# Kernel optimization log

Measured on AMD Instinct MI355X. Metric: run time of the kernel, lower is better.

Reference implementation:

```python
import jax, jax.numpy as jnp
import numpy as np

MODEL = 2048
LATENT = 512
POS = 1024
NH = 16
HD = MODEL // NH        # 128
PHD = POS // NH         # 64
THETA = 50000.0


def _rope_tables(S, dim, base=THETA):
    inv_freq = 1.0 / (base ** (jnp.arange(0, dim, 2, dtype=jnp.float32) / dim))
    t = jnp.arange(S, dtype=jnp.float32)
    freqs = jnp.outer(t, inv_freq)                  # [S, dim/2]
    emb = jnp.concatenate([freqs, freqs], axis=-1)  # [S, dim]
    return jnp.cos(emb), jnp.sin(emb)


def _rotate_half(x):
    h = x.shape[-1] // 2
    return jnp.concatenate([-x[..., h:], x[..., :h]], axis=-1)


def _apply_rope(x, cos, sin):
    # x: [..., S, dim]; cos/sin: [S, dim]
    return x * cos + _rotate_half(x) * sin


def setup_inputs() -> dict:
    key = jax.random.key(0)
    ks = jax.random.split(key, 16)
    std = 0.02
    d = {
        'x':      jax.random.normal(ks[0], (2, 2048, MODEL), jnp.float32),
        'w_qkv':  jax.random.normal(ks[1], (MODEL, 3 * LATENT), jnp.float32) * std,
        'b_qkv':  jnp.zeros((3 * LATENT,), jnp.float32),
        'w_qup':  jax.random.normal(ks[2], (LATENT, MODEL), jnp.float32) * std,
        'b_qup':  jnp.zeros((MODEL,), jnp.float32),
        'w_kup':  jax.random.normal(ks[3], (LATENT, MODEL), jnp.float32) * std,
        'b_kup':  jnp.zeros((MODEL,), jnp.float32),
        'w_vup':  jax.random.normal(ks[4], (LATENT, MODEL), jnp.float32) * std,
        'b_vup':  jnp.zeros((MODEL,), jnp.float32),
        'w_qpos': jax.random.normal(ks[5], (LATENT, POS), jnp.float32) * std,
        'b_qpos': jnp.zeros((POS,), jnp.float32),
        'w_kpos': jax.random.normal(ks[6], (MODEL, PHD), jnp.float32) * std,
        'b_kpos': jnp.zeros((PHD,), jnp.float32),
        'w_o':    jax.random.normal(ks[7], (MODEL, MODEL), jnp.float32) * std,
        'b_o':    jnp.zeros((MODEL,), jnp.float32),
    }
    return d


def reference(x, w_qkv, b_qkv, w_qup, b_qup, w_kup, b_kup, w_vup, b_vup,
              w_qpos, b_qpos, w_kpos, b_kpos, w_o, b_o):
    B, S, _ = x.shape
    # fused down-projection into shared latent
    latent_qkv = x @ w_qkv + b_qkv                       # [B,S,3L]
    lq, lk, lv = jnp.split(latent_qkv, 3, axis=-1)       # each [B,S,L]

    cos, sin = _rope_tables(S, PHD)

    # decoupled positional key (shared across heads), RoPE on sub-slice
    pos_k = x @ w_kpos + b_kpos                          # [B,S,PHD]
    pos_k = _apply_rope(pos_k, cos, sin)

    # up-projections
    q = (lq @ w_qup + b_qup).reshape(B, S, NH, HD).transpose(0, 2, 1, 3)
    k = (lk @ w_kup + b_kup).reshape(B, S, NH, HD).transpose(0, 2, 1, 3)
    v = (lv @ w_vup + b_vup).reshape(B, S, NH, HD).transpose(0, 2, 1, 3)

    pos_q = (lq @ w_qpos + b_qpos).reshape(B, S, NH, PHD).transpose(0, 2, 1, 3)
    pos_q = _apply_rope(pos_q, cos, sin)                 # [B,NH,S,PHD]

    pos_kh = jnp.broadcast_to(pos_k[:, None], (B, NH, S, PHD))
    q = jnp.concatenate([q, pos_q], axis=-1)             # [B,NH,S,HD+PHD]
    k = jnp.concatenate([k, pos_kh], axis=-1)

    scale = 1.0 / jnp.sqrt(jnp.asarray(HD + PHD, x.dtype))
    scores = jnp.einsum('bhqd,bhkd->bhqk', q, k) * scale
    causal = jnp.tril(jnp.ones((S, S), bool))
    scores = jnp.where(causal, scores, jnp.finfo(scores.dtype).min)
    p = jax.nn.softmax(scores, axis=-1)
    attn = jnp.einsum('bhqk,bhkd->bhqd', p, v)           # [B,NH,S,HD]
    attn = attn.transpose(0, 2, 1, 3).reshape(B, S, MODEL)
    return attn @ w_o + b_o
```

## Files before the change

### kernel.cpp

```cpp
#include <hip/hip_runtime.h>
#include <cstdint>
#include <cstddef>

typedef __bf16 bf16x8 __attribute__((ext_vector_type(8)));
typedef float  f32x4  __attribute__((ext_vector_type(4)));
typedef unsigned short us8 __attribute__((ext_vector_type(8)));
typedef unsigned short us4 __attribute__((ext_vector_type(4)));

__device__ __forceinline__ unsigned short f2bf(float f) {
  union { float f; unsigned u; } v; v.f = f;
  unsigned r = v.u + 0x7FFFu + ((v.u >> 16) & 1u);
  return (unsigned short)(r >> 16);
}
__device__ __forceinline__ float b2f(unsigned short h) {
  union { unsigned u; float f; } v; v.u = ((unsigned)h) << 16;
  return v.f;
}
__device__ __forceinline__ f32x4 mfma16(bf16x8 a, bf16x8 b, f32x4 c) {
  return __builtin_amdgcn_mfma_f32_16x16x32_bf16(a, b, c, 0, 0, 0);
}
__device__ __forceinline__ void gl_lds16(const unsigned short* g, unsigned short* l) {
  __builtin_amdgcn_global_load_lds(
      (const __attribute__((address_space(1))) void*)g,
      (__attribute__((address_space(3))) void*)l, 16, 0, 0);
}

__global__ void prep_all_kernel(const float* __restrict__ b_qkv,
                                const float* __restrict__ b_kpos,
                                const float* __restrict__ b_qup,
                                const float* __restrict__ b_qpos,
                                float* __restrict__ bias1,
                                float* __restrict__ bias2q,
                                float* __restrict__ costab,
                                float* __restrict__ sintab,
                                unsigned short* __restrict__ wB1,
                                const float* __restrict__ w_qkv,
                                const float* __restrict__ w_kpos,
                                const float* __restrict__ w_qup,
                                const float* __restrict__ w_qpos,
                                const float* __restrict__ w_kup,
                                const float* __restrict__ w_vup,
                                const float* __restrict__ w_o,
                                unsigned short* __restrict__ wB2q,
                                unsigned short* __restrict__ wB2k,
                                unsigned short* __restrict__ wB2v,
                                unsigned short* __restrict__ wBo,
                                int* __restrict__ counters) {
  __shared__ float tile[32][33];
  int blk = blockIdx.x;
  if (blk < 512) {
    int i = blk * 256 + threadIdx.x;
    if (i < 65536) {
      int s = i >> 5, f = i & 31;
      float inv = powf(50000.0f, -(float)f / 32.0f);
      float a = (float)s * inv;
      costab[i] = cosf(a);
      sintab[i] = sinf(a);
    }
    if (i < 2048) bias1[i] = (i < 1536) ? b_qkv[i] : (i < 1600 ? b_kpos[i - 1536] : 0.0f);
    if (i < 3072) bias2q[i] = (i < 2048) ? b_qup[i] : b_qpos[i - 2048];
    for (int jj = 0; jj < 7; ++jj)
      wB1[(size_t)1600 * 2048 + (size_t)jj * 131072 + i] = 0;
    if (i < 64) counters[i] = 0;
    return;
  }
  const float* in;
  unsigned short* out;
  int ldin, ldo, nx, j;
  if (blk < 3584)      { j = blk - 512;  in = w_qkv;  ldin = 1536; out = wB1;                        ldo = 2048; nx = 48; }
  else if (blk < 3712) { j = blk - 3584; in = w_kpos; ldin = 64;   out = wB1 + (size_t)1536 * 2048;  ldo = 2048; nx = 2;  }
  else if (blk < 4736) { j = blk - 3712; in = w_qup;  ldin = 2048; out = wB2q;                       ldo = 512;  nx = 64; }
  else if (blk < 5248) { j = blk - 4736; in = w_qpos; ldin = 1024; out = wB2q + (size_t)2048 * 512;  ldo = 512;  nx = 32; }
  else if (blk < 6272) { j = blk - 5248; in = w_kup;  ldin = 2048; out = wB2k;                       ldo = 512;  nx = 64; }
  else if (blk < 7296) { j = blk - 6272; in = w_vup;  ldin = 2048; out = wB2v;                       ldo = 512;  nx = 64; }
  else                 { j = blk - 7296; in = w_o;    ldin = 2048; out = wBo;                        ldo = 2048; nx = 64; }
  int c0 = (j % nx) * 32, r0 = (j / nx) * 32;
  int tx = threadIdx.x & 31, ty = threadIdx.x >> 5;
  for (int jj = 0; jj < 4; ++jj)
    tile[ty + jj * 8][tx] = in[(size_t)(r0 + ty + jj * 8) * ldin + c0 + tx];
  __syncthreads();
  for (int jj = 0; jj < 4; ++jj)
    out[(size_t)(c0 + ty + jj * 8) * ldo + r0 + tx] = f2bf(tile[tx][ty + jj * 8]);
}

__device__ __forceinline__ void xcd_decode(int nx, int& bx, int& by) {
  int bid = blockIdx.x, nwg = gridDim.x;
  int cpx = nwg >> 3;
  int wg = (bid & 7) * cpx + (bid >> 3);
  bx = wg % nx;
  by = wg / nx;
}

template <int OUT_MODE>
__global__ __launch_bounds__(256, 2)
void gemm_bt_kernel(const unsigned short* __restrict__ A, int lda,
                    const unsigned short* __restrict__ Bt, int ldb,
                    void* __restrict__ Cout, int ldc,
                    const float* __restrict__ bias, int K, int nx) {
  __shared__ unsigned short smem[32768];
  int tid = threadIdx.x;
  int wave = tid >> 6, lane = tid & 63;
  int g = lane >> 4, r = lane & 15;
  int wr = wave >> 1, wc = wave & 1;
  int bx, by;
  xcd_decode(nx, bx, by);
  long brow = (long)by * 128, bcol = (long)bx * 128;

  int srowl = lane >> 3;
  int sw = ((lane & 7) ^ (srowl & 7)) * 8;
  const unsigned short* Abase = A + (brow + wave * 32 + srowl) * (long)lda + sw;
  const unsigned short* Bbase = Bt + (bcol + wave * 32 + srowl) * (long)ldb + sw;

  f32x4 acc[4][4];
  for (int mi = 0; mi < 4; ++mi)
    for (int ni = 0; ni < 4; ++ni)
      acc[mi][ni] = f32x4{0.f, 0.f, 0.f, 0.f};

  auto stage = [&](int buf, int k0) {
    unsigned short* ab = smem + buf * 16384;
    unsigned short* bb = ab + 8192;
    for (int c = 0; c < 4; ++c) {
      gl_lds16(Abase + (size_t)c * 8 * lda + k0, ab + (wave * 32 + c * 8) * 64);
      gl_lds16(Bbase + (size_t)c * 8 * ldb + k0, bb + (wave * 32 + c * 8) * 64);
    }
  };

  int rx = (r & 7) << 4;
  int nt = K >> 6;

  stage(0, 0);
  for (int t = 0; t < nt; ++t) {
    if (t + 1 < nt) {
      stage((t + 1) & 1, (t + 1) << 6);
      asm volatile("s_waitcnt vmcnt(8)" ::: "memory");
    } else {
      asm volatile("s_waitcnt vmcnt(0)" ::: "memory");
    }
    __builtin_amdgcn_sched_barrier(0);
    __builtin_amdgcn_s_barrier();
    __builtin_amdgcn_sched_barrier(0);
    const char* Ab = (const char*)(smem + (t & 1) * 16384);
    const char* Bb = Ab + 16384;
    for (int kk = 0; kk < 2; ++kk) {
      bf16x8 af[4], bfv[4];
      for (int mi = 0; mi < 4; ++mi)
        af[mi] = *(const bf16x8*)(Ab + (size_t)(wr * 64 + mi * 16 + r) * 128 +
                                  ((kk * 64 + g * 16) ^ rx));
      for (int ni = 0; ni < 4; ++ni)
        bfv[ni] = *(const bf16x8*)(Bb + (size_t)(wc * 64 + ni * 16 + r) * 128 +
                                   ((kk * 64 + g * 16) ^ rx));
      for (int mi = 0; mi < 4; ++mi)
        for (int ni = 0; ni < 4; ++ni)
          acc[mi][ni] = mfma16(af[mi], bfv[ni], acc[mi][ni]);
    }
    __builtin_amdgcn_sched_barrier(0);
    __builtin_amdgcn_s_barrier();
  }

  if (OUT_MODE == 2) {
    for (int mi = 0; mi < 4; ++mi)
      for (int ni = 0; ni < 4; ++ni) {
        int col = wc * 64 + ni * 16 + r;
        float bv = bias[bcol + col];
        int rowb = wr * 64 + mi * 16 + g * 4;
        for (int i = 0; i < 4; ++i)
          smem[col * 136 + rowb + i] = f2bf(acc[mi][ni][i] + bv);
      }
    __syncthreads();
    int col = tid >> 1, half = tid & 1;
    int bh = (int)(brow >> 11) * 16 + (int)(bcol >> 7);
    unsigned short* outp = (unsigned short*)Cout +
                           ((size_t)bh * 128 + col) * 2048 + (brow & 2047);
    for (int j = 0; j < 8; ++j) {
      int row0 = half * 64 + j * 8;
      *(us8*)(outp + row0) = *(const us8*)&smem[col * 136 + row0];
    }
    return;
  }

  for (int mi = 0; mi < 4; ++mi)
    for (int ni = 0; ni < 4; ++ni) {
      long col = bcol + wc * 64 + ni * 16 + r;
      float bv = bias ? bias[col] : 0.0f;
      long rowb = brow + wr * 64 + mi * 16 + g * 4;
      for (int i = 0; i < 4; ++i) {
        float v = acc[mi][ni][i] + bv;
        if (OUT_MODE == 1)
          ((float*)Cout)[(rowb + i) * (long)ldc + col] = v;
        else
          ((unsigned short*)Cout)[(rowb + i) * (long)ldc + col] = f2bf(v);
      }
    }
}

__global__ __launch_bounds__(256, 2)
void gemm_a32_kernel(const float* __restrict__ A, int lda,
                     const unsigned short* __restrict__ Bt, int ldb,
                     unsigned short* __restrict__ Cout, int ldc,
                     const float* __restrict__ bias, int K, int nx) {
  __shared__ unsigned short smem[32768];
  int tid = threadIdx.x;
  int wave = tid >> 6, lane = tid & 63;
  int g = lane >> 4, r = lane & 15;
  int wr = wave >> 1, wc = wave & 1;
  int bx, by;
  xcd_decode(nx, bx, by);
  long brow = (long)by * 128, bcol = (long)bx * 128;

  int f4c = tid & 15, row0 = tid >> 4;
  int ablk = f4c >> 1, asub = (f4c & 1) * 8;
  const float4* Ag = (const float4*)(A + (brow + row0) * (size_t)lda) + f4c;

  int srowl = lane >> 3;
  int sw = ((lane & 7) ^ (srowl & 7)) * 8;
  const unsigned short* Bbase = Bt + (bcol + wave * 32 + srowl) * (long)ldb + sw;

  f32x4 acc[4][4];
  for (int mi = 0; mi < 4; ++mi)
    for (int ni = 0; ni < 4; ++ni)
      acc[mi][ni] = f32x4{0.f, 0.f, 0.f, 0.f};

  auto stage_b = [&](int buf, int k0) {
    unsigned short* bb = smem + 16384 + buf * 8192;
    for (int c = 0; c < 4; ++c)
      gl_lds16(Bbase + (size_t)c * 8 * ldb + k0, bb + (wave * 32 + c * 8) * 64);
  };

  int rx = (r & 7) << 4;
  int nt = K >> 6;

  float4 areg[8];
#pragma unroll
  for (int s = 0; s < 8; ++s) areg[s] = Ag[(size_t)s * 8192];
  stage_b(0, 0);

  for (int t = 0; t < nt; ++t) {
    char* alds = (char*)(smem + (t & 1) * 8192);
#pragma unroll
    for (int s = 0; s < 8; ++s) {
      us4 hv;
      hv[0] = f2bf(areg[s].x); hv[1] = f2bf(areg[s].y);
      hv[2] = f2bf(areg[s].z); hv[3] = f2bf(areg[s].w);
      int row = row0 + s * 16;
      *(us4*)(alds + row * 128 + ((ablk ^ (row & 7)) << 4) + asub) = hv;
    }
    asm volatile("s_waitcnt vmcnt(0)" ::: "memory");
    asm volatile("s_waitcnt lgkmcnt(0)" ::: "memory");
    __builtin_amdgcn_sched_barrier(0);
    __builtin_amdgcn_s_barrier();
    __builtin_amdgcn_sched_barrier(0);
    if (t + 1 < nt) {
      int k1 = (t + 1) << 6;
#pragma unroll
      for (int s = 0; s < 8; ++s) areg[s] = Ag[(size_t)s * 8192 + (k1 >> 2)];
      stage_b((t + 1) & 1, k1);
    }
    const char* Ab = (const char*)(smem + (t & 1) * 8192);
    const char* Bb = (const char*)(smem + 16384 + (t & 1) * 8192);
    for (int kk = 0; kk < 2; ++kk) {
      bf16x8 af[4], bfv[4];
      for (int mi = 0; mi < 4; ++mi)
        af[mi] = *(const bf16x8*)(Ab + (size_t)(wr * 64 + mi * 16 + r) * 128 +
                                  ((kk * 64 + g * 16) ^ rx));
      for (int ni = 0; ni < 4; ++ni)
        bfv[ni] = *(const bf16x8*)(Bb + (size_t)(wc * 64 + ni * 16 + r) * 128 +
                                   ((kk * 64 + g * 16) ^ rx));
      for (int mi = 0; mi < 4; ++mi)
        for (int ni = 0; ni < 4; ++ni)
          acc[mi][ni] = mfma16(af[mi], bfv[ni], acc[mi][ni]);
    }
    __builtin_amdgcn_sched_barrier(0);
    __builtin_amdgcn_s_barrier();
  }

  for (int mi = 0; mi < 4; ++mi)
    for (int ni = 0; ni < 4; ++ni) {
      long col = bcol + wc * 64 + ni * 16 + r;
      float bv = bias[col];
      long rowb = brow + wr * 64 + mi * 16 + g * 4;
      for (int i = 0; i < 4; ++i)
        Cout[(rowb + i) * (long)ldc + col] = f2bf(acc[mi][ni][i] + bv);
    }
}

__global__ void rope_kernel(const unsigned short* __restrict__ tmp_q,
                            const unsigned short* __restrict__ latext,
                            const float* __restrict__ costab,
                            const float* __restrict__ sintab,
                            unsigned short* __restrict__ posqr,
                            unsigned short* __restrict__ poskr) {
  int idx = blockIdx.x * 256 + threadIdx.x;
  const unsigned short* src;
  unsigned short* dst;
  int s, dp0;
  if (idx < 524288) {
    int rowA = idx >> 7, rem = idx & 127;
    int h = rem >> 3;
    dp0 = (rem & 7) * 8;
    s = rowA & 2047;
    src = tmp_q + (size_t)rowA * 3072 + 2048 + h * 64;
    dst = posqr + (size_t)rowA * 1024 + h * 64 + dp0;
  } else if (idx < 557056) {
    int j = idx - 524288;
    int rowA = j >> 3;
    dp0 = (j & 7) * 8;
    s = rowA & 2047;
    src = latext + (size_t)rowA * 2048 + 1536;
    dst = poskr + (size_t)rowA * 64 + dp0;
  } else {
    return;
  }
  us8 x1 = *(const us8*)(src + dp0);
  us8 x2 = *(const us8*)(src + (dp0 ^ 32));
  int f0 = dp0 & 31;
  const float* cp = costab + s * 32 + f0;
  const float* sp = sintab + s * 32 + f0;
  bool low = dp0 < 32;
  us8 o;
  for (int e = 0; e < 8; ++e) {
    float a = b2f(x1[e]), b = b2f(x2[e]);
    float v = low ? (a * cp[e] - b * sp[e]) : (a * cp[e] + b * sp[e]);
    o[e] = f2bf(v);
  }
  *(us8*)dst = o;
}

__device__ __forceinline__ void task_decode(int t, int& qt, int& seg, int& bh) {
  if (t < 1024) {
    qt = 31 - (t >> 7); int rem = t & 127; seg = rem >> 5; bh = rem & 31;
  } else if (t < 1792) {
    int t2 = t - 1024; int qi = t2 / 96; int rem = t2 - qi * 96;
    qt = 23 - qi; seg = rem >> 5; bh = rem & 31;
  } else if (t < 2304) {
    int t3 = t - 1792; qt = 15 - (t3 >> 6); int rem = t3 & 63; seg = rem >> 5; bh = rem & 31;
  } else {
    int t4 = t - 2304; qt = 7 - (t4 >> 5); seg = 0; bh = t4 & 31;
  }
}
__device__ __forceinline__ int task_slot(int qt, int seg, int bh) {
  if (qt >= 24) return (31 - qt) * 128 + seg * 32 + bh;
  if (qt >= 16) return 1024 + (23 - qt) * 96 + seg * 32 + bh;
  return 1792 + (15 - qt) * 64 + seg * 32 + bh;
}

__global__ __launch_bounds__(256, 2)
void flash_kernel(const unsigned short* __restrict__ tmp_q,
                  const unsigned short* __restrict__ tmp_k,
                  const unsigned short* __restrict__ posqr,
                  const unsigned short* __restrict__ poskr,
                  const unsigned short* __restrict__ vT,
                  unsigned short* __restrict__ ob,
                  unsigned short* __restrict__ Opart,
                  float* __restrict__ mlbuf,
                  int* __restrict__ counter) {
  const int S = 2048;
  int tid = threadIdx.x, wave = tid >> 6, lane = tid & 63;
  int g = lane >> 4, r = lane & 15;
  const float sl2 = 1.44269504f / 13.8564064605510183f;
  const float DEFER = 96.0f;

  __shared__ unsigned short Klds[32 * 192];
  __shared__ unsigned short Vlds[128 * 32];
  __shared__ unsigned short Plds[4][16][40];
  __shared__ int s_tile;
  char* Kb = (char*)Klds;
  char* Vb = (char*)Vlds;
  int rx7 = (r & 7) << 4, rx3 = (r & 3) << 4;

  us8 onesu;
  for (int e = 0; e < 8; ++e) onesu[e] = 0x3F80;
  bf16x8 ones = *(const bf16x8*)&onesu;

  int kn_row[2], kn_seg[2];
  for (int j = 0; j < 2; ++j) {
    int slot = j * 256 + tid;
    kn_row[j] = slot >> 4;
    kn_seg[j] = slot & 15;
  }
  int kr_row = tid >> 3, kr_seg = tid & 7;
  int v_row[2], v_seg[2];
  for (int j = 0; j < 2; ++j) {
    int slot = j * 256 + tid;
    v_row[j] = slot >> 2;
    v_seg[j] = slot & 3;
  }

  for (;;) {
    if (tid == 0) s_tile = atomicAdd(counter, 1);
    __syncthreads();
    int t = s_tile;
    if (t >= 2560) return;
    int qt, seg, bh;
    task_decode(t, qt, seg, bh);
    int b = bh >> 4, h = bh & 15;
    int qbase = qt * 64;
    int cbeg = seg * 16;
    int cend = min(cbeg + 16, 2 * (qt + 1));
    size_t rb = (size_t)b * 2048;

    const unsigned short* kpn = tmp_k + rb * 2048 + h * 128;
    const unsigned short* kpr = poskr + rb * 64;
    const unsigned short* vp = vT + (size_t)bh * 128 * S;

    bf16x8 qf[6];
    {
      size_t qrowA = rb + qbase + wave * 16 + r;
      const unsigned short* qn = tmp_q + qrowA * 3072 + h * 128 + g * 8;
      for (int c = 0; c < 4; ++c) qf[c] = *(const bf16x8*)(qn + c * 32);
      const unsigned short* qr_ = posqr + qrowA * 1024 + h * 64 + g * 8;
      qf[4] = *(const bf16x8*)(qr_);
      qf[5] = *(const bf16x8*)(qr_ + 32);
    }

    f32x4 acc[8];
    for (int d = 0; d < 8; ++d) acc[d] = f32x4{0.f, 0.f, 0.f, 0.f};
    f32x4 lacc = {0.f, 0.f, 0.f, 0.f};
    float m_r[4];
    for (int i = 0; i < 4; ++i) m_r[i] = -3.0e38f;

    us8 kreg[2], krope, vreg[2];
    {
      int kv0 = cbeg * 32;
      for (int j = 0; j < 2; ++j)
        kreg[j] = *(const us8*)(kpn + (size_t)(kv0 + kn_row[j]) * 2048 + kn_seg[j] * 8);
      krope = *(const us8*)(kpr + (size_t)(kv0 + kr_row) * 64 + kr_seg * 8);
      for (int j = 0; j < 2; ++j)
        vreg[j] = *(const us8*)(vp + (size_t)v_row[j] * S + kv0 + v_seg[j] * 8);
    }

    for (int ch = cbeg; ch < cend; ++ch) {
      for (int j = 0; j < 2; ++j)
        *(us8*)(Kb + (size_t)kn_row[j] * 384 +
                ((kn_seg[j] ^ (kn_row[j] & 7)) << 4)) = kreg[j];
      *(us8*)(Kb + (size_t)kr_row * 384 +
              (((16 + kr_seg) ^ (kr_row & 7)) << 4)) = krope;
      for (int j = 0; j < 2; ++j)
        *(us8*)(Vb + (size_t)v_row[j] * 64 +
                ((v_seg[j] ^ (v_row[j] & 3)) << 4)) = vreg[j];
      asm volatile("s_waitcnt lgkmcnt(0)" ::: "memory");
      __builtin_amdgcn_sched_barrier(0);
      __builtin_amdgcn_s_barrier();
      __builtin_amdgcn_sched_barrier(0);
      if (ch + 1 < cend) {
        int kv1 = (ch + 1) * 32;
        for (int j = 0; j < 2; ++j)
          kreg[j] = *(const us8*)(kpn + (size_t)(kv1 + kn_row[j]) * 2048 + kn_seg[j] * 8);
        krope = *(const us8*)(kpr + (size_t)(kv1 + kr_row) * 64 + kr_seg * 8);
        for (int j = 0; j < 2; ++j)
          vreg[j] = *(const us8*)(vp + (size_t)v_row[j] * S + kv1 + v_seg[j] * 8);
      }
      int kv0 = ch * 32;

      f32x4 sc0 = {0.f, 0.f, 0.f, 0.f}, sc1 = {0.f, 0.f, 0.f, 0.f};
      __builtin_amdgcn_s_setprio(1);
      for (int c = 0; c < 6; ++c) {
        bf16x8 kf0 = *(const bf16x8*)(Kb + (size_t)r * 384 + (((c * 4 + g) << 4) ^ rx7));
        sc0 = mfma16(qf[c], kf0, sc0);
      }
      for (int c = 0; c < 6; ++c) {
        bf16x8 kf1 = *(const bf16x8*)(Kb + (size_t)(16 + r) * 384 + (((c * 4 + g) << 4) ^ rx7));
        sc1 = mfma16(qf[c], kf1, sc1);
      }
      __builtin_amdgcn_s_setprio(0);

      int qi_min = qbase + wave * 16;
      if (kv0 + 31 > qi_min) {
        int kj0 = kv0 + r, kj1 = kv0 + 16 + r;
        int qi0 = qi_min + g * 4;
        for (int i = 0; i < 4; ++i) {
          if (kj0 > qi0 + i) sc0[i] = -1e30f;
          if (kj1 > qi0 + i) sc1[i] = -1e30f;
        }
      }

      float tl[4];
      bool ok = true;
      for (int i = 0; i < 4; ++i) {
        tl[i] = fmaxf(sc0[i], sc1[i]);
        ok = ok && (tl[i] - m_r[i] <= DEFER);
      }
      if (!__all(ok)) {
        for (int i = 0; i < 4; ++i) {
          float tm = tl[i];
          for (int off = 1; off < 16; off <<= 1) tm = fmaxf(tm, __shfl_xor(tm, off, 64));
          float mnew = fmaxf(m_r[i], tm);
          float corr = exp2f((m_r[i] - mnew) * sl2);
          lacc[i] *= corr;
          for (int d = 0; d < 8; ++d) acc[d][i] *= corr;
          m_r[i] = mnew;
        }
      }
      float p0[4], p1[4];
      for (int i = 0; i < 4; ++i) {
        p0[i] = exp2f((sc0[i] - m_r[i]) * sl2);
        p1[i] = exp2f((sc1[i] - m_r[i]) * sl2);
      }

      for (int i = 0; i < 4; ++i) {
        Plds[wave][g * 4 + i][r] = f2bf(p0[i]);
        Plds[wave][g * 4 + i][16 + r] = f2bf(p1[i]);
      }
      bf16x8 pa = *(const bf16x8*)&Plds[wave][r][g * 8];
      __builtin_amdgcn_s_setprio(1);
      lacc = mfma16(pa, ones, lacc);
      for (int dt = 0; dt < 8; ++dt) {
        bf16x8 vf = *(const bf16x8*)(Vb + (size_t)(dt * 16 + r) * 64 + ((g << 4) ^ rx3));
        acc[dt] = mfma16(pa, vf, acc[dt]);
      }
      __builtin_amdgcn_s_setprio(0);
      __builtin_amdgcn_sched_barrier(0);
      __builtin_amdgcn_s_barrier();
    }

    if (qt <= 7) {
      for (int i = 0; i < 4; ++i) {
        float inv = 1.0f / lacc[i];
        int row = qbase + wave * 16 + g * 4 + i;
        size_t base = (rb + row) * 2048 + h * 128;
        for (int dt = 0; dt < 8; ++dt)
          ob[base + dt * 16 + r] = f2bf(acc[dt][i] * inv);
      }
    } else {
      unsigned short* op = Opart + (size_t)t * 8192;
      for (int i = 0; i < 4; ++i) {
        int row = wave * 16 + g * 4 + i;
        for (int dt = 0; dt < 8; ++dt)
          op[row * 128 + dt * 16 + r] = f2bf(acc[dt][i]);
        if (r == 0) {
          mlbuf[(size_t)t * 128 + row * 2]     = m_r[i];
          mlbuf[(size_t)t * 128 + row * 2 + 1] = lacc[i];
        }
      }
    }
  }
}

__global__ void merge_kernel(const unsigned short* __restrict__ Opart,
                             const float* __restrict__ mlbuf,
                             unsigned short* __restrict__ ob) {
  int qt = 8 + (blockIdx.x >> 5), bh = blockIdx.x & 31;
  int b = bh >> 4, h = bh & 15;
  int tid = threadIdx.x;
  int row = tid >> 2, c0 = (tid & 3) * 32;
  const float sl2 = 1.44269504f / 13.8564064605510183f;
  int ns = (qt >= 24) ? 4 : (qt >= 16 ? 3 : 2);

  size_t slot[4];
  float m[4], l[4], w[4];
  float M = -3.0e38f;
#pragma unroll
  for (int j = 0; j < 4; ++j) {
    if (j < ns) {
      slot[j] = task_slot(qt, j, bh);
      m[j] = mlbuf[slot[j] * 128 + row * 2];
      l[j] = mlbuf[slot[j] * 128 + row * 2 + 1];
      M = fmaxf(M, m[j]);
    }
  }
  float L = 0.f;
#pragma unroll
  for (int j = 0; j < 4; ++j)
    if (j < ns) { w[j] = exp2f((m[j] - M) * sl2); L += w[j] * l[j]; }
  float invL = 1.f / L;
#pragma unroll
  for (int j = 0; j < 4; ++j) if (j < ns) w[j] *= invL;

  float o[32];
#pragma unroll
  for (int e = 0; e < 32; ++e) o[e] = 0.f;
#pragma unroll
  for (int j = 0; j < 4; ++j) {
    if (j < ns) {
      const unsigned short* pp = Opart + slot[j] * 8192 + row * 128 + c0;
      for (int blk = 0; blk < 4; ++blk) {
        us8 v = *(const us8*)(pp + blk * 8);
        for (int e = 0; e < 8; ++e) o[blk * 8 + e] += w[j] * b2f(v[e]);
      }
    }
  }
  size_t obase = ((size_t)b * 2048 + qt * 64 + row) * 2048 + h * 128 + c0;
  for (int blk = 0; blk < 4; ++blk) {
    us8 st;
    for (int e = 0; e < 8; ++e) st[e] = f2bf(o[blk * 8 + e]);
    *(us8*)(ob + obase + blk * 8) = st;
  }
}

extern "C" void kernel_launch(void* const* d_in, const int* in_sizes, int n_in,
                              void* d_out, int out_size, void* d_ws, size_t ws_size,
                              hipStream_t stream) {
  const float* x      = (const float*)d_in[0];
  const float* w_qkv  = (const float*)d_in[1];
  const float* b_qkv  = (const float*)d_in[2];
  const float* w_qup  = (const float*)d_in[3];
  const float* b_qup  = (const float*)d_in[4];
  const float* w_kup  = (const float*)d_in[5];
  const float* b_kup  = (const float*)d_in[6];
  const float* w_vup  = (const float*)d_in[7];
  const float* b_vup  = (const float*)d_in[8];
  const float* w_qpos = (const float*)d_in[9];
  const float* b_qpos = (const float*)d_in[10];
  const float* w_kpos = (const float*)d_in[11];
  const float* b_kpos = (const float*)d_in[12];
  const float* w_o    = (const float*)d_in[13];
  const float* b_o    = (const float*)d_in[14];
  (void)in_sizes; (void)n_in; (void)out_size; (void)ws_size;

  char* ws = (char*)d_ws;
  size_t off = 0;
  auto alloc = [&](size_t bytes) -> char* {
    char* p = ws + off;
    off += (bytes + 255) & ~(size_t)255;
    return p;
  };

  unsigned short* wB1    = (unsigned short*)alloc(8388608);
  unsigned short* wB2q   = (unsigned short*)alloc(3145728);
  unsigned short* wB2k   = (unsigned short*)alloc(2097152);
  unsigned short* wB2v   = (unsigned short*)alloc(2097152);
  unsigned short* wBo    = (unsigned short*)alloc(8388608);
  float*          bias1  = (float*)alloc(2048 * 4);
  float*          bias2q = (float*)alloc(3072 * 4);
  float*          costab = (float*)alloc(262144);
  float*          sintab = (float*)alloc(262144);
  unsigned short* latext = (unsigned short*)alloc(16777216);
  unsigned short* tmp_q  = (unsigned short*)alloc(25165824);
  unsigned short* tmp_k  = (unsigned short*)alloc(16777216);
  unsigned short* vTbuf  = (unsigned short*)alloc(16777216);
  unsigned short* posqr  = (unsigned short*)alloc(8388608);
  unsigned short* poskr  = (unsigned short*)alloc(524288);
  unsigned short* Opart  = (unsigned short*)alloc(41943040);
  float*          mlbuf  = (float*)alloc(1310720);
  int*            counter= (int*)alloc(256);
  unsigned short* attnb  = (unsigned short*)alloc(16777216);

  prep_all_kernel<<<11392, 256, 0, stream>>>(b_qkv, b_kpos, b_qup, b_qpos,
                                             bias1, bias2q, costab, sintab, wB1,
                                             w_qkv, w_kpos, w_qup, w_qpos, w_kup,
                                             w_vup, w_o, wB2q, wB2k, wB2v, wBo,
                                             counter);
  gemm_a32_kernel<<<512, 256, 0, stream>>>(x, 2048, wB1, 2048,
                                           latext, 2048, bias1, 2048, 16);
  gemm_bt_kernel<0><<<768, 256, 0, stream>>>(latext, 2048, wB2q, 512,
                                             tmp_q, 3072, bias2q, 512, 24);
  gemm_bt_kernel<0><<<512, 256, 0, stream>>>(latext + 512, 2048, wB2k, 512,
                                             tmp_k, 2048, b_kup, 512, 16);
  gemm_bt_kernel<2><<<512, 256, 0, stream>>>(latext + 1024, 2048, wB2v, 512,
                                             vTbuf, 2048, b_vup, 512, 16);
  rope_kernel<<<2176, 256, 0, stream>>>(tmp_q, latext, costab, sintab, posqr, poskr);
  flash_kernel<<<1280, 256, 0, stream>>>(tmp_q, tmp_k, posqr, poskr, vTbuf,
                                         attnb, Opart, mlbuf, counter);
  merge_kernel<<<768, 256, 0, stream>>>(Opart, mlbuf, attnb);
  gemm_bt_kernel<1><<<512, 256, 0, stream>>>(attnb, 2048, wBo, 2048,
                                             d_out, 2048, b_o, 2048, 16);
}
```

Measured before the change: 282.8 us.

## Process two 32-key chunks per LDS stage in flash attention

Doubles the K/V shared-memory tile from 32 to 64 keys. Each barrier-separated stage now runs two score/softmax/PV sub-iterations, and the next 64 keys are prefetched into registers. The V tile uses a 128-byte row stride with an 8-way XOR swizzle to match. This halves the number of block barriers and global-load rounds per tile and keeps more loads in flight. The cost is more LDS and more prefetch registers per thread, which may lower occupancy. The persistent grid is also reduced from 1280 to 768 blocks.

Measured after the change: 288.5 us. +2.0%, slower.

```diff
diff --git a/kernel.cpp b/kernel.cpp
--- a/kernel.cpp
+++ b/kernel.cpp
@@ -359,30 +359,35 @@
   const float sl2 = 1.44269504f / 13.8564064605510183f;
   const float DEFER = 96.0f;
 
-  __shared__ unsigned short Klds[32 * 192];
-  __shared__ unsigned short Vlds[128 * 32];
+  __shared__ unsigned short Klds[64 * 192];
+  __shared__ unsigned short Vlds[128 * 64];
   __shared__ unsigned short Plds[4][16][40];
   __shared__ int s_tile;
   char* Kb = (char*)Klds;
   char* Vb = (char*)Vlds;
-  int rx7 = (r & 7) << 4, rx3 = (r & 3) << 4;
+  int rx7 = (r & 7) << 4;
 
   us8 onesu;
   for (int e = 0; e < 8; ++e) onesu[e] = 0x3F80;
   bf16x8 ones = *(const bf16x8*)&onesu;
 
-  int kn_row[2], kn_seg[2];
-  for (int j = 0; j < 2; ++j) {
+  int kn_row[4], kn_seg[4];
+  for (int j = 0; j < 4; ++j) {
     int slot = j * 256 + tid;
     kn_row[j] = slot >> 4;
     kn_seg[j] = slot & 15;
   }
-  int kr_row = tid >> 3, kr_seg = tid & 7;
-  int v_row[2], v_seg[2];
+  int kr_row[2], kr_seg[2];
   for (int j = 0; j < 2; ++j) {
     int slot = j * 256 + tid;
-    v_row[j] = slot >> 2;
-    v_seg[j] = slot & 3;
+    kr_row[j] = slot >> 3;
+    kr_seg[j] = slot & 7;
+  }
+  int v_row[4], v_seg[4];
+  for (int j = 0; j < 4; ++j) {
+    int slot = j * 256 + tid;
+    v_row[j] = slot >> 3;
+    v_seg[j] = slot & 7;
   }
 
   for (;;) {
@@ -418,96 +423,107 @@
     float m_r[4];
     for (int i = 0; i < 4; ++i) m_r[i] = -3.0e38f;
 
-    us8 kreg[2], krope, vreg[2];
+    us8 kreg[4], krope[2], vreg[4];
     {
       int kv0 = cbeg * 32;
+      for (int j = 0; j < 4; ++j)
+        kreg[j] = *(const us8*)(kpn + (size_t)(kv0 + kn_row[j]) * 2048 + kn_seg[j] * 8);
       for (int j = 0; j < 2; ++j)
-        kreg[j] = *(const us8*)(kpn + (size_t)(kv0 + kn_row[j]) * 2048 + kn_seg[j] * 8);
-      krope = *(const us8*)(kpr + (size_t)(kv0 + kr_row) * 64 + kr_seg * 8);
-      for (int j = 0; j < 2; ++j)
+        krope[j] = *(const us8*)(kpr + (size_t)(kv0 + kr_row[j]) * 64 + kr_seg[j] * 8);
+      for (int j = 0; j < 4; ++j)
         vreg[j] = *(const us8*)(vp + (size_t)v_row[j] * S + kv0 + v_seg[j] * 8);
     }
 
-    for (int ch = cbeg; ch < cend; ++ch) {
-      for (int j = 0; j < 2; ++j)
+    for (int ch = cbeg; ch < cend; ch += 2) {
+      for (int j = 0; j < 4; ++j)
         *(us8*)(Kb + (size_t)kn_row[j] * 384 +
                 ((kn_seg[j] ^ (kn_row[j] & 7)) << 4)) = kreg[j];
-      *(us8*)(Kb + (size_t)kr_row * 384 +
-              (((16 + kr_seg) ^ (kr_row & 7)) << 4)) = krope;
       for (int j = 0; j < 2; ++j)
-        *(us8*)(Vb + (size_t)v_row[j] * 64 +
-                ((v_seg[j] ^ (v_row[j] & 3)) << 4)) = vreg[j];
+        *(us8*)(Kb + (size_t)kr_row[j] * 384 +
+                (((16 + kr_seg[j]) ^ (kr_row[j] & 7)) << 4)) = krope[j];
+      for (int j = 0; j < 4; ++j)
+        *(us8*)(Vb + (size_t)v_row[j] * 128 +
+                ((v_seg[j] ^ (v_row[j] & 7)) << 4)) = vreg[j];
       asm volatile("s_waitcnt lgkmcnt(0)" ::: "memory");
       __builtin_amdgcn_sched_barrier(0);
       __builtin_amdgcn_s_barrier();
       __builtin_amdgcn_sched_barrier(0);
-      if (ch + 1 < cend) {
-        int kv1 = (ch + 1) * 32;
+      if (ch + 2 < cend) {
+        int kv1 = (ch + 2) * 32;
+        for (int j = 0; j < 4; ++j)
+          kreg[j] = *(const us8*)(kpn + (size_t)(kv1 + kn_row[j]) * 2048 + kn_seg[j] * 8);
         for (int j = 0; j < 2; ++j)
-          kreg[j] = *(const us8*)(kpn + (size_t)(kv1 + kn_row[j]) * 2048 + kn_seg[j] * 8);
-        krope = *(const us8*)(kpr + (size_t)(kv1 + kr_row) * 64 + kr_seg * 8);
-        for (int j = 0; j < 2; ++j)
+          krope[j] = *(const us8*)(kpr + (size_t)(kv1 + kr_row[j]) * 64 + kr_seg[j] * 8);
+        for (int j = 0; j < 4; ++j)
           vreg[j] = *(const us8*)(vp + (size_t)v_row[j] * S + kv1 + v_seg[j] * 8);
       }
-      int kv0 = ch * 32;
-
-      f32x4 sc0 = {0.f, 0.f, 0.f, 0.f}, sc1 = {0.f, 0.f, 0.f, 0.f};
-      __builtin_amdgcn_s_setprio(1);
-      for (int c = 0; c < 6; ++c) {
-        bf16x8 kf0 = *(const bf16x8*)(Kb + (size_t)r * 384 + (((c * 4 + g) << 4) ^ rx7));
-        sc0 = mfma16(qf[c], kf0, sc0);
+
+#pragma unroll
+      for (int sub = 0; sub < 2; ++sub) {
+        int kv0 = (ch + sub) * 32;
+        int krow0 = sub * 32;
+
+        f32x4 sc0 = {0.f, 0.f, 0.f, 0.f}, sc1 = {0.f, 0.f, 0.f, 0.f};
+        __builtin_amdgcn_s_setprio(1);
+        for (int c = 0; c < 6; ++c) {
+          bf16x8 kf0 = *(const bf16x8*)(Kb + (size_t)(krow0 + r) * 384 +
+                                        (((c * 4 + g) << 4) ^ rx7));
+          sc0 = mfma16(qf[c], kf0, sc0);
+        }
+        for (int c = 0; c < 6; ++c) {
+          bf16x8 kf1 = *(const bf16x8*)(Kb + (size_t)(krow0 + 16 + r) * 384 +
+                                        (((c * 4 + g) << 4) ^ rx7));
+          sc1 = mfma16(qf[c], kf1, sc1);
+        }
+        __builtin_amdgcn_s_setprio(0);
+
+        int qi_min = qbase + wave * 16;
+        if (kv0 + 31 > qi_min) {
+          int kj0 = kv0 + r, kj1 = kv0 + 16 + r;
+          int qi0 = qi_min + g * 4;
+          for (int i = 0; i < 4; ++i) {
+            if (kj0 > qi0 + i) sc0[i] = -1e30f;
+            if (kj1 > qi0 + i) sc1[i] = -1e30f;
+          }
+        }
+
+        float tl[4];
+        bool ok = true;
+        for (int i = 0; i < 4; ++i) {
+          tl[i] = fmaxf(sc0[i], sc1[i]);
+          ok = ok && (tl[i] - m_r[i] <= DEFER);
+        }
+        if (!__all(ok)) {
+          for (int i = 0; i < 4; ++i) {
+            float tm = tl[i];
+            for (int off = 1; off < 16; off <<= 1) tm = fmaxf(tm, __shfl_xor(tm, off, 64));
+            float mnew = fmaxf(m_r[i], tm);
+            float corr = exp2f((m_r[i] - mnew) * sl2);
+            lacc[i] *= corr;
+            for (int d = 0; d < 8; ++d) acc[d][i] *= corr;
+            m_r[i] = mnew;
+          }
+        }
+        float p0[4], p1[4];
+        for (int i = 0; i < 4; ++i) {
+          p0[i] = exp2f((sc0[i] - m_r[i]) * sl2);
+          p1[i] = exp2f((sc1[i] - m_r[i]) * sl2);
+        }
+
+        for (int i = 0; i < 4; ++i) {
+          Plds[wave][g * 4 + i][r] = f2bf(p0[i]);
+          Plds[wave][g * 4 + i][16 + r] = f2bf(p1[i]);
+        }
+        bf16x8 pa = *(const bf16x8*)&Plds[wave][r][g * 8];
+        __builtin_amdgcn_s_setprio(1);
+        lacc = mfma16(pa, ones, lacc);
+        for (int dt = 0; dt < 8; ++dt) {
+          bf16x8 vf = *(const bf16x8*)(Vb + (size_t)(dt * 16 + r) * 128 +
+                                       (((sub * 4 + g) << 4) ^ rx7));
+          acc[dt] = mfma16(pa, vf, acc[dt]);
+        }
+        __builtin_amdgcn_s_setprio(0);
       }
-      for (int c = 0; c < 6; ++c) {
-        bf16x8 kf1 = *(const bf16x8*)(Kb + (size_t)(16 + r) * 384 + (((c * 4 + g) << 4) ^ rx7));
-        sc1 = mfma16(qf[c], kf1, sc1);
-      }
-      __builtin_amdgcn_s_setprio(0);
-
-      int qi_min = qbase + wave * 16;
-      if (kv0 + 31 > qi_min) {
-        int kj0 = kv0 + r, kj1 = kv0 + 16 + r;
-        int qi0 = qi_min + g * 4;
-        for (int i = 0; i < 4; ++i) {
-          if (kj0 > qi0 + i) sc0[i] = -1e30f;
-          if (kj1 > qi0 + i) sc1[i] = -1e30f;
-        }
-      }
-
-      float tl[4];
-      bool ok = true;
-      for (int i = 0; i < 4; ++i) {
-        tl[i] = fmaxf(sc0[i], sc1[i]);
-        ok = ok && (tl[i] - m_r[i] <= DEFER);
-      }
-      if (!__all(ok)) {
-        for (int i = 0; i < 4; ++i) {
-          float tm = tl[i];
-          for (int off = 1; off < 16; off <<= 1) tm = fmaxf(tm, __shfl_xor(tm, off, 64));
-          float mnew = fmaxf(m_r[i], tm);
-          float corr = exp2f((m_r[i] - mnew) * sl2);
-          lacc[i] *= corr;
-          for (int d = 0; d < 8; ++d) acc[d][i] *= corr;
-          m_r[i] = mnew;
-        }
-      }
-      float p0[4], p1[4];
-      for (int i = 0; i < 4; ++i) {
-        p0[i] = exp2f((sc0[i] - m_r[i]) * sl2);
-        p1[i] = exp2f((sc1[i] - m_r[i]) * sl2);
-      }
-
-      for (int i = 0; i < 4; ++i) {
-        Plds[wave][g * 4 + i][r] = f2bf(p0[i]);
-        Plds[wave][g * 4 + i][16 + r] = f2bf(p1[i]);
-      }
-      bf16x8 pa = *(const bf16x8*)&Plds[wave][r][g * 8];
-      __builtin_amdgcn_s_setprio(1);
-      lacc = mfma16(pa, ones, lacc);
-      for (int dt = 0; dt < 8; ++dt) {
-        bf16x8 vf = *(const bf16x8*)(Vb + (size_t)(dt * 16 + r) * 64 + ((g << 4) ^ rx3));
-        acc[dt] = mfma16(pa, vf, acc[dt]);
-      }
-      __builtin_amdgcn_s_setprio(0);
       __builtin_amdgcn_sched_barrier(0);
       __builtin_amdgcn_s_barrier();
     }
@@ -648,8 +664,8 @@
   gemm_bt_kernel<2><<<512, 256, 0, stream>>>(latext + 1024, 2048, wB2v, 512,
                                              vTbuf, 2048, b_vup, 512, 16);
   rope_kernel<<<2176, 256, 0, stream>>>(tmp_q, latext, costab, sintab, posqr, poskr);
-  flash_kernel<<<1280, 256, 0, stream>>>(tmp_q, tmp_k, posqr, poskr, vTbuf,
-                                         attnb, Opart, mlbuf, counter);
+  flash_kernel<<<768, 256, 0, stream>>>(tmp_q, tmp_k, posqr, poskr, vTbuf,
+                                        attnb, Opart, mlbuf, counter);
   merge_kernel<<<768, 256, 0, stream>>>(Opart, mlbuf, attnb);
   gemm_bt_kernel<1><<<512, 256, 0, stream>>>(attnb, 2048, wBo, 2048,
                                              d_out, 2048, b_o, 2048, 16);
```
